# Optimization experiments

Hardware: AMD Instinct MI355X
Metric: run time of the kernel (lower is better)

Reference implementation:

```python
import jax, jax.numpy as jnp
import numpy as np

THRESH = 0.5
DECAY = 0.2
N_NODES = 39
T = 2000
K_HOPS = 3


def setup_inputs() -> dict:
    key = jax.random.key(0)
    ks = jax.random.split(key, 10)
    x = jax.random.normal(ks[0], (N_NODES, 2, T), dtype=jnp.float32)
    edge_index = jax.random.randint(ks[1], (2, 156), 0, N_NODES)
    # TAGConv(2, 64, K=3): (K+1) bias-free hop weights + single bias
    W_conv = jax.random.normal(ks[2], (K_HOPS + 1, 2, 64), dtype=jnp.float32) * 0.3
    b_conv = jax.random.normal(ks[3], (64,), dtype=jnp.float32) * 0.05
    W1 = jax.random.normal(ks[4], (N_NODES * 64, 128), dtype=jnp.float32) * 0.02
    b1 = jax.random.normal(ks[5], (128,), dtype=jnp.float32) * 0.02
    W2 = jax.random.normal(ks[6], (128, 256), dtype=jnp.float32) * 0.08
    b2 = jax.random.normal(ks[7], (256,), dtype=jnp.float32) * 0.02
    W3 = jax.random.normal(ks[8], (256, 36), dtype=jnp.float32) * 0.06
    b3 = jax.random.normal(ks[9], (36,), dtype=jnp.float32) * 0.02
    return {"x": x, "edge_index": edge_index, "W_conv": W_conv, "b_conv": b_conv,
            "W1": W1, "b1": b1, "W2": W2, "b2": b2, "W3": W3, "b3": b3}


def _norm_adj(edge_index, dtype):
    # PyG gcn_norm without self loops: A_hat = D^-1/2 A D^-1/2, message flows row->col
    row, col = edge_index[0], edge_index[1]
    A = jnp.zeros((N_NODES, N_NODES), dtype).at[col, row].add(1.0)
    deg = A.sum(axis=1)
    dinv = jnp.where(deg > 0, deg ** -0.5, 0.0).astype(dtype)
    return dinv[:, None] * A * dinv[None, :]


def reference(x, edge_index, W_conv, b_conv, W1, b1, W2, b2, W3, b3):
    A_hat = _norm_adj(edge_index, x.dtype)

    def spike(m):
        return (m > THRESH).astype(m.dtype)

    def step(carry, xt):
        c1m, c1s, h1m, h1s, h2m, h2s, h3m, h3s, acc = carry
        # TAGConv: sum_k (A_hat^k xt) @ W_k + bias   [39,64]
        h = xt
        conv = h @ W_conv[0]
        for k in range(1, K_HOPS + 1):
            h = A_hat @ h
            conv = conv + h @ W_conv[k]
        conv = conv + b_conv
        c1m = c1m * DECAY * (1.0 - c1s) + conv
        c1s = spike(c1m)
        f = c1s.reshape(-1)  # [2496]
        h1m = h1m * DECAY * (1.0 - h1s) + f @ W1 + b1
        h1s = spike(h1m)
        h2m = h2m * DECAY * (1.0 - h2s) + h1s @ W2 + b2
        h2s = spike(h2m)
        h3m = h3m * DECAY * (1.0 - h3s) + h2s @ W3 + b3
        h3s = spike(h3m)
        return (c1m, c1s, h1m, h1s, h2m, h2s, h3m, h3s, acc + h3s), None

    z = lambda s: jnp.zeros(s, x.dtype)
    init = (z((N_NODES, 64)), z((N_NODES, 64)), z((128,)), z((128,)),
            z((256,)), z((256,)), z((36,)), z((36,)), z((36,)))
    xs = jnp.moveaxis(x, -1, 0)  # [T, 39, 2]
    carry, _ = jax.lax.scan(step, init, xs)
    return carry[-1] / x.shape[-1]
```

## Files before the change

kernel.cpp:

```cpp
#include <hip/hip_runtime.h>

#define T 2000
#define K1N 2496
#define K2 4992
#define TL 48
#define WL 16
#define NCHB 42
#define MAXNZ 24

using short8 = __attribute__((ext_vector_type(8))) short;
using floatx4 = __attribute__((ext_vector_type(4))) float;

__device__ __forceinline__ unsigned bf16_rne(float v) {
    unsigned u = __float_as_uint(v);
    return (u + 0x7FFFu + ((u >> 16) & 1u)) >> 16;
}
__device__ __forceinline__ unsigned packhl(float w) {
    unsigned hi = bf16_rne(w);
    float r = w - __uint_as_float(hi << 16);
    unsigned lo = bf16_rne(r);
    return (hi & 0xFFFFu) | (lo << 16);
}

template<int LEN, bool WRITE>
__device__ __forceinline__ void subtile(
        const float* __restrict__ x, unsigned char* __restrict__ FS,
        float* bufA, float* bufB, float* feat,
        const float2* alist, const int* nnzr,
        int tid, int i0, int iloc, int n, bool vn,
        int ts, const float* wv, float bias, float& m, float& s) {
    constexpr int GC = LEN / 8;
    for (int e = tid; e < 78 * LEN; e += 256) {
        int r = e / LEN, tt = e - r * LEN;
        int t = ts + tt;
        bufA[r * TL + tt] = (t < T) ? x[r * T + t] : 0.f;
    }
    __syncthreads();
    for (int e = tid; e < 8 * LEN; e += 256) {
        int lr = e / LEN, tt = e - lr * LEN;
        int gr = i0 * 2 + lr;
        float v = (gr < 78) ? bufA[gr * TL + tt] : 0.f;
        feat[(((lr >> 1) * TL) + tt) * 8 + (lr & 1)] = v;
    }
    for (int e = tid; e < 78 * GC; e += 256) {
        int r = e / GC, g = e - r * GC;
        int ii = r >> 1, c = r & 1;
        float acc[8];
        #pragma unroll
        for (int u = 0; u < 8; ++u) acc[u] = 0.f;
        int nz = nnzr[ii];
        const float2* lp = &alist[ii * MAXNZ];
        int cg = c * (TL * 4) + g * 32;
        for (int q = 0; q < nz; ++q) {
            float2 av = lp[q];
            const float* xp = (const float*)((const char*)bufA + (__float_as_int(av.y) + cg));
            float a = av.x;
            float4 x0 = *(const float4*)xp;
            float4 x1 = *(const float4*)(xp + 4);
            acc[0] += a * x0.x; acc[1] += a * x0.y; acc[2] += a * x0.z; acc[3] += a * x0.w;
            acc[4] += a * x1.x; acc[5] += a * x1.y; acc[6] += a * x1.z; acc[7] += a * x1.w;
        }
        float* dp = &bufB[r * TL + g * 8];
        *(float4*)dp = *(float4*)&acc[0];
        *(float4*)(dp + 4) = *(float4*)&acc[4];
    }
    __syncthreads();
    for (int e = tid; e < 8 * LEN; e += 256) {
        int lr = e / LEN, tt = e - lr * LEN;
        int gr = i0 * 2 + lr;
        float v = (gr < 78) ? bufB[gr * TL + tt] : 0.f;
        feat[(((lr >> 1) * TL) + tt) * 8 + 2 + (lr & 1)] = v;
    }
    for (int e = tid; e < 78 * GC; e += 256) {
        int r = e / GC, g = e - r * GC;
        int ii = r >> 1, c = r & 1;
        float acc[8];
        #pragma unroll
        for (int u = 0; u < 8; ++u) acc[u] = 0.f;
        int nz = nnzr[ii];
        const float2* lp = &alist[ii * MAXNZ];
        int cg = c * (TL * 4) + g * 32;
        for (int q = 0; q < nz; ++q) {
            float2 av = lp[q];
            const float* xp = (const float*)((const char*)bufB + (__float_as_int(av.y) + cg));
            float a = av.x;
            float4 x0 = *(const float4*)xp;
            float4 x1 = *(const float4*)(xp + 4);
            acc[0] += a * x0.x; acc[1] += a * x0.y; acc[2] += a * x0.z; acc[3] += a * x0.w;
            acc[4] += a * x1.x; acc[5] += a * x1.y; acc[6] += a * x1.z; acc[7] += a * x1.w;
        }
        float* dp = &bufA[r * TL + g * 8];
        *(float4*)dp = *(float4*)&acc[0];
        *(float4*)(dp + 4) = *(float4*)&acc[4];
    }
    __syncthreads();
    for (int e = tid; e < 8 * LEN; e += 256) {
        int lr = e / LEN, tt = e - lr * LEN;
        int gr = i0 * 2 + lr;
        float v = (gr < 78) ? bufA[gr * TL + tt] : 0.f;
        feat[(((lr >> 1) * TL) + tt) * 8 + 4 + (lr & 1)] = v;
    }
    for (int e = tid; e < 8 * GC; e += 256) {
        int lr = e / GC, g = e - lr * GC;
        int gi = i0 + (lr >> 1), c = lr & 1, il = lr >> 1;
        float acc[8];
        #pragma unroll
        for (int u = 0; u < 8; ++u) acc[u] = 0.f;
        if (gi < 39) {
            int nz = nnzr[gi];
            const float2* lp = &alist[gi * MAXNZ];
            int cg = c * (TL * 4) + g * 32;
            for (int q = 0; q < nz; ++q) {
                float2 av = lp[q];
                const float* xp = (const float*)((const char*)bufA + (__float_as_int(av.y) + cg));
                float a = av.x;
                float4 x0 = *(const float4*)xp;
                float4 x1 = *(const float4*)(xp + 4);
                acc[0] += a * x0.x; acc[1] += a * x0.y; acc[2] += a * x0.z; acc[3] += a * x0.w;
                acc[4] += a * x1.x; acc[5] += a * x1.y; acc[6] += a * x1.z; acc[7] += a * x1.w;
            }
        }
        #pragma unroll
        for (int u = 0; u < 8; ++u)
            feat[((il * TL) + g * 8 + u) * 8 + 6 + c] = acc[u];
    }
    __syncthreads();
    for (int tg = 0; tg < LEN; tg += 8) {
        float4 f0a[8], f1a[8];
        #pragma unroll
        for (int u = 0; u < 8; ++u) {
            const float4* fp = (const float4*)&feat[((iloc * TL) + tg + u) * 8];
            f0a[u] = fp[0];
            f1a[u] = fp[1];
        }
        #pragma unroll
        for (int u = 0; u < 8; ++u) {
            float acc = 0.f;
            acc += wv[0] * f0a[u].x; acc += wv[1] * f0a[u].y;
            acc += wv[2] * f0a[u].z; acc += wv[3] * f0a[u].w;
            acc += wv[4] * f1a[u].x; acc += wv[5] * f1a[u].y;
            acc += wv[6] * f1a[u].z; acc += wv[7] * f1a[u].w;
            float v = acc + bias;
            m = m * 0.2f * (1.f - s) + v;
            s = (m > 0.5f) ? 1.f : 0.f;
            if (WRITE && vn) {
                int t = ts + tg + u;
                if (t < T) FS[t * K1N + n] = (unsigned char)(s != 0.f);
            }
        }
    }
    __syncthreads();
}

__global__ __launch_bounds__(256) void conv_scan(const float* __restrict__ x,
        const int* __restrict__ ei, const float* __restrict__ Wc,
        const float* __restrict__ bc, unsigned char* __restrict__ FS,
        const float* __restrict__ W1, unsigned* __restrict__ W1t,
        float* __restrict__ out) {
    __shared__ float ah[1560];
    __shared__ float2 alist[39 * MAXNZ];
    __shared__ int nnzr[40];
    __shared__ float bufA[78 * TL];
    __shared__ float bufB[78 * TL];
    __shared__ float feat[4 * TL * 8];
    int tid = threadIdx.x;
    int nb = blockIdx.x, ch = blockIdx.y;
    int bl = ch * 10 + nb;

    if (bl == 0 && tid < 36) out[tid] = 0.f;

    for (int u = tid; u < 1521; u += 256) ah[u] = 0.f;
    __syncthreads();
    if (tid < 156) atomicAdd(&ah[ei[156 + tid] * 39 + ei[tid]], 1.f);
    __syncthreads();
    if (tid < 39) {
        float d = 0.f;
        for (int u = 0; u < 39; ++u) d += ah[tid * 39 + u];
        ah[1521 + tid] = (d > 0.f) ? (1.f / sqrtf(d)) : 0.f;
    }
    __syncthreads();
    for (int u = tid; u < 1521; u += 256) {
        int i = u / 39, j = u - i * 39;
        ah[u] = (ah[1521 + i] * ah[u]) * ah[1521 + j];
    }
    __syncthreads();
    if (tid < 39) {
        int cnt = 0;
        for (int m = 0; m < 39; ++m) {
            float v = ah[tid * 39 + m];
            if (v != 0.f && cnt < MAXNZ) {
                alist[tid * MAXNZ + cnt] = make_float2(v, __int_as_float((2 * m) * TL * 4));
                ++cnt;
            }
        }
        nnzr[tid] = cnt;
    }
    __syncthreads();

    int t0 = ch * TL;
    int i0 = nb * 4;
    int iloc = tid >> 6, j = tid & 63;
    int n = nb * 256 + tid;
    bool vn = (i0 + iloc) < 39;
    float wv[8], bias;
    #pragma unroll
    for (int q = 0; q < 8; ++q) wv[q] = Wc[q * 64 + j];
    bias = bc[j];
    float m = 0.f, s = 0.f;

    if (t0 >= WL)
        subtile<WL, false>(x, FS, bufA, bufB, feat, alist, nnzr,
                           tid, i0, iloc, n, vn, t0 - WL, wv, bias, m, s);
    subtile<TL, true>(x, FS, bufA, bufB, feat, alist, nnzr,
                      tid, i0, iloc, n, vn, t0, wv, bias, m, s);

    const int total = 128 * K1N;
    for (int f = bl * 256 + tid; f < total; f += 420 * 256) {
        int k = f >> 7, jj = f & 127;
        W1t[jj * K1N + k] = packhl(W1[f]);
    }
}

__global__ __launch_bounds__(256) void gemm1(const unsigned char* __restrict__ FS,
        const short* __restrict__ W1t, float* __restrict__ F1p) {
    __shared__ short As[32 * 72];
    __shared__ short Ws[128 * 72];
    int tid = threadIdx.x;
    int t0 = blockIdx.x * 32;
    int ks = blockIdx.y;
    int lane = tid & 63, wvi = tid >> 6;
    int j0 = wvi * 32;
    int row = lane & 15, quad = lane >> 4;
    floatx4 a00 = {0.f, 0.f, 0.f, 0.f};
    floatx4 a01 = a00, a10 = a00, a11 = a00;
    int kb = ks * 416, kb2 = ks * 832;
    int sm = tid >> 3, sb4 = (tid & 7) * 4;
    int gt = t0 + sm;
    int jjv[4], kov[4];
    #pragma unroll
    for (int u = 0; u < 4; ++u) {
        int aid = u * 256 + tid;
        jjv[u] = aid >> 3;
        kov[u] = (aid & 7) * 8;
    }
    unsigned u4 = 0;
    short8 wr0, wr1, wr2, wr3;
    if (gt < T) u4 = *(const unsigned*)&FS[gt * K1N + kb + sb4];
    wr0 = *(const short8*)&W1t[jjv[0] * K2 + kb2 + kov[0]];
    wr1 = *(const short8*)&W1t[jjv[1] * K2 + kb2 + kov[1]];
    wr2 = *(const short8*)&W1t[jjv[2] * K2 + kb2 + kov[2]];
    wr3 = *(const short8*)&W1t[jjv[3] * K2 + kb2 + kov[3]];
    for (int c = 0; c < 13; ++c) {
        uint4 dd;
        dd.x = (u4 & 0x000000FFu) ? 0x3F803F80u : 0u;
        dd.y = (u4 & 0x0000FF00u) ? 0x3F803F80u : 0u;
        dd.z = (u4 & 0x00FF0000u) ? 0x3F803F80u : 0u;
        dd.w = (u4 & 0xFF000000u) ? 0x3F803F80u : 0u;
        *(uint4*)&As[sm * 72 + sb4 * 2] = dd;
        *(short8*)&Ws[jjv[0] * 72 + kov[0]] = wr0;
        *(short8*)&Ws[jjv[1] * 72 + kov[1]] = wr1;
        *(short8*)&Ws[jjv[2] * 72 + kov[2]] = wr2;
        *(short8*)&Ws[jjv[3] * 72 + kov[3]] = wr3;
        __syncthreads();
        unsigned u4n = 0;
        short8 wn0, wn1, wn2, wn3;
        if (c < 12) {
            if (gt < T) u4n = *(const unsigned*)&FS[gt * K1N + kb + (c + 1) * 32 + sb4];
            wn0 = *(const short8*)&W1t[jjv[0] * K2 + kb2 + (c + 1) * 64 + kov[0]];
            wn1 = *(const short8*)&W1t[jjv[1] * K2 + kb2 + (c + 1) * 64 + kov[1]];
            wn2 = *(const short8*)&W1t[jjv[2] * K2 + kb2 + (c + 1) * 64 + kov[2]];
            wn3 = *(const short8*)&W1t[jjv[3] * K2 + kb2 + (c + 1) * 64 + kov[3]];
        }
        #pragma unroll
        for (int sh = 0; sh < 2; ++sh) {
            int k0 = sh * 32 + quad * 8;
            short8 fa0 = *(const short8*)&As[row * 72 + k0];
            short8 fa1 = *(const short8*)&As[(row + 16) * 72 + k0];
            short8 fb0 = *(const short8*)&Ws[(j0 + row) * 72 + k0];
            short8 fb1 = *(const short8*)&Ws[(j0 + 16 + row) * 72 + k0];
            a00 = __builtin_amdgcn_mfma_f32_16x16x32_bf16(fa0, fb0, a00, 0, 0, 0);
            a01 = __builtin_amdgcn_mfma_f32_16x16x32_bf16(fa0, fb1, a01, 0, 0, 0);
            a10 = __builtin_amdgcn_mfma_f32_16x16x32_bf16(fa1, fb0, a10, 0, 0, 0);
            a11 = __builtin_amdgcn_mfma_f32_16x16x32_bf16(fa1, fb1, a11, 0, 0, 0);
        }
        __syncthreads();
        if (c < 12) { u4 = u4n; wr0 = wn0; wr1 = wn1; wr2 = wn2; wr3 = wn3; }
    }
    #pragma unroll
    for (int r = 0; r < 4; ++r) {
        int m0 = quad * 4 + r;
        int t = t0 + m0;
        if (t < T) {
            F1p[t * 768 + ks * 128 + j0 + row] = a00[r];
            F1p[t * 768 + ks * 128 + j0 + 16 + row] = a01[r];
        }
        int t2 = t0 + 16 + m0;
        if (t2 < T) {
            F1p[t2 * 768 + ks * 128 + j0 + row] = a10[r];
            F1p[t2 * 768 + ks * 128 + j0 + 16 + row] = a11[r];
        }
    }
}

__global__ __launch_bounds__(256) void h1_gemm2(const float* __restrict__ F1p,
        const float* __restrict__ b1, const float* __restrict__ W2,
        float* __restrict__ G2) {
    __shared__ float AT[128 * 8];
    int tid = threadIdx.x;
    int t0 = blockIdx.x * 8;
    if (tid < 128) {
        int n = tid;
        int hs = t0 - 16; if (hs < 0) hs = 0;
        float b = b1[n];
        float m = 0.f, s = 0.f;
        for (int tg = hs; tg < t0 + 8; tg += 4) {
            float vb[4][6];
            #pragma unroll
            for (int u = 0; u < 4; ++u)
                #pragma unroll
                for (int q = 0; q < 6; ++q)
                    vb[u][q] = F1p[(tg + u) * 768 + q * 128 + n];
            #pragma unroll
            for (int u = 0; u < 4; ++u) {
                float v = 0.f;
                #pragma unroll
                for (int q = 0; q < 6; ++q) v += vb[u][q];
                v += b;
                m = m * 0.2f * (1.f - s) + v;
                s = (m > 0.5f) ? 1.f : 0.f;
                int t = tg + u;
                if (t >= t0) AT[n * 8 + (t - t0)] = s;
            }
        }
    }
    __syncthreads();
    int j = tid;
    float acc[8] = {0.f};
    #pragma unroll 4
    for (int k = 0; k < 128; ++k) {
        float w = W2[k * 256 + j];
        float4 q0 = *(const float4*)&AT[k * 8 + 0];
        float4 q1 = *(const float4*)&AT[k * 8 + 4];
        acc[0] += q0.x * w; acc[1] += q0.y * w; acc[2] += q0.z * w; acc[3] += q0.w * w;
        acc[4] += q1.x * w; acc[5] += q1.y * w; acc[6] += q1.z * w; acc[7] += q1.w * w;
    }
    #pragma unroll
    for (int tt = 0; tt < 8; ++tt) G2[(t0 + tt) * 256 + j] = acc[tt];
}

__global__ __launch_bounds__(256) void tail(const float* __restrict__ G2,
        const float* __restrict__ b2, const float* __restrict__ W3,
        const float* __restrict__ b3, float* __restrict__ out) {
    __shared__ float w3t[36 * 260];
    __shared__ unsigned char S2[52 * 260];
    __shared__ float G3[52 * 36];
    int tid = threadIdx.x;
    int t0 = blockIdx.x * 25;
    int gs = t0 - 25; if (gs < 0) gs = 0;
    int hs = gs - 25; if (hs < 0) hs = 0;
    int L3 = t0 + 25 - gs;
    #pragma unroll
    for (int u = 0; u < 9; ++u) {
        int f = u * 1024 + tid * 4;
        float4 wq = *(const float4*)&W3[f];
        int k0 = f / 36, j0 = f - k0 * 36;
        float wv[4] = {wq.x, wq.y, wq.z, wq.w};
        #pragma unroll
        for (int q = 0; q < 4; ++q) {
            int k = (j0 + q >= 36) ? k0 + 1 : k0;
            int jj = (j0 + q >= 36) ? (j0 + q - 36) : (j0 + q);
            w3t[jj * 260 + k] = wv[q];
        }
    }
    {
        int n = tid;
        float b = b2[n];
        float m = 0.f, s = 0.f;
        for (int base = hs; base < t0 + 25; base += 25) {
            float vb[25];
            #pragma unroll
            for (int u = 0; u < 25; ++u) vb[u] = G2[(base + u) * 256 + n];
            #pragma unroll
            for (int u = 0; u < 25; ++u) {
                float v = vb[u] + b;
                m = m * 0.2f * (1.f - s) + v;
                s = (m > 0.5f) ? 1.f : 0.f;
                int t = base + u;
                if (t >= gs) S2[(t - gs) * 260 + n] = (unsigned char)(s != 0.f);
            }
        }
    }
    __syncthreads();
    for (int e = tid; e < 36 * 13; e += 256) {
        int jj = e / 13, g = e - (e / 13) * 13;
        int tb = g * 4;
        if (tb >= L3) continue;
        float ac0 = 0.f, ac1 = 0.f, ac2 = 0.f, ac3 = 0.f;
        const unsigned char* r0 = &S2[tb * 260];
        for (int k = 0; k < 256; k += 4) {
            float4 w = *(const float4*)&w3t[jj * 260 + k];
            uchar4 q0 = *(const uchar4*)&r0[k];
            uchar4 q1 = *(const uchar4*)&r0[260 + k];
            uchar4 q2 = *(const uchar4*)&r0[520 + k];
            uchar4 q3 = *(const uchar4*)&r0[780 + k];
            ac0 += (float)q0.x * w.x + (float)q0.y * w.y + (float)q0.z * w.z + (float)q0.w * w.w;
            ac1 += (float)q1.x * w.x + (float)q1.y * w.y + (float)q1.z * w.z + (float)q1.w * w.w;
            ac2 += (float)q2.x * w.x + (float)q2.y * w.y + (float)q2.z * w.z + (float)q2.w * w.w;
            ac3 += (float)q3.x * w.x + (float)q3.y * w.y + (float)q3.z * w.z + (float)q3.w * w.w;
        }
        G3[tb * 36 + jj] = ac0;
        if (tb + 1 < L3) G3[(tb + 1) * 36 + jj] = ac1;
        if (tb + 2 < L3) G3[(tb + 2) * 36 + jj] = ac2;
        if (tb + 3 < L3) G3[(tb + 3) * 36 + jj] = ac3;
    }
    __syncthreads();
    if (tid < 36) {
        int n = tid;
        float b = b3[n];
        float m = 0.f, s = 0.f;
        int cnt = 0;
        for (int t = gs; t < t0 + 25; ++t) {
            float v = G3[(t - gs) * 36 + n] + b;
            m = m * 0.2f * (1.f - s) + v;
            s = (m > 0.5f) ? 1.f : 0.f;
            if (t >= t0) cnt += (s != 0.f) ? 1 : 0;
        }
        atomicAdd(&out[n], (float)cnt * 0.0005f);
    }
}

extern "C" void kernel_launch(void* const* d_in, const int* in_sizes, int n_in,
                              void* d_out, int out_size, void* d_ws, size_t ws_size,
                              hipStream_t stream) {
    const float* x  = (const float*)d_in[0];
    const int*   ei = (const int*)d_in[1];
    const float* Wc = (const float*)d_in[2];
    const float* bc = (const float*)d_in[3];
    const float* W1 = (const float*)d_in[4];
    const float* b1 = (const float*)d_in[5];
    const float* W2 = (const float*)d_in[6];
    const float* b2 = (const float*)d_in[7];
    const float* W3 = (const float*)d_in[8];
    const float* b3 = (const float*)d_in[9];
    float* out = (float*)d_out;

    float* w = (float*)d_ws;
    float* F1p = w;                       w += (size_t)T * 768;
    float* G2  = w;                       w += (size_t)T * 256;
    unsigned* W1t = (unsigned*)w;         w += 128 * K1N;
    unsigned char* FS = (unsigned char*)w;

    conv_scan<<<dim3(10, NCHB), 256, 0, stream>>>(x, ei, Wc, bc, FS, W1, W1t, out);
    gemm1<<<dim3(63, 6), 256, 0, stream>>>(FS, (const short*)W1t, F1p);
    h1_gemm2<<<250, 256, 0, stream>>>(F1p, b1, W2, G2);
    tail<<<80, 256, 0, stream>>>(G2, b2, W3, b3, out);
}
```

Before: 145.6 us.

## Split graph-hop computation into separate kernel, removing redundant per-block hop recomputation

```diff
diff --git a/kernel.cpp b/kernel.cpp
--- a/kernel.cpp
+++ b/kernel.cpp
@@ -6,6 +6,7 @@
 #define TL 48
 #define WL 16
 #define NCHB 42
+#define TLA 8
 #define MAXNZ 24
 
 using short8 = __attribute__((ext_vector_type(8))) short;
@@ -22,35 +23,69 @@
     return (hi & 0xFFFFu) | (lo << 16);
 }
 
-template<int LEN, bool WRITE>
-__device__ __forceinline__ void subtile(
-        const float* __restrict__ x, unsigned char* __restrict__ FS,
-        float* bufA, float* bufB, float* feat,
-        const float2* alist, const int* nnzr,
-        int tid, int i0, int iloc, int n, bool vn,
-        int ts, const float* wv, float bias, float& m, float& s) {
-    constexpr int GC = LEN / 8;
-    for (int e = tid; e < 78 * LEN; e += 256) {
-        int r = e / LEN, tt = e - r * LEN;
-        int t = ts + tt;
-        bufA[r * TL + tt] = (t < T) ? x[r * T + t] : 0.f;
-    }
-    __syncthreads();
-    for (int e = tid; e < 8 * LEN; e += 256) {
-        int lr = e / LEN, tt = e - lr * LEN;
-        int gr = i0 * 2 + lr;
-        float v = (gr < 78) ? bufA[gr * TL + tt] : 0.f;
-        feat[(((lr >> 1) * TL) + tt) * 8 + (lr & 1)] = v;
-    }
-    for (int e = tid; e < 78 * GC; e += 256) {
-        int r = e / GC, g = e - r * GC;
+__global__ __launch_bounds__(256) void hops(const float* __restrict__ x,
+        const int* __restrict__ ei, float* __restrict__ Fg,
+        const float* __restrict__ W1, unsigned* __restrict__ W1t,
+        float* __restrict__ out) {
+    __shared__ float ah[1560];
+    __shared__ float2 alist[39 * MAXNZ];
+    __shared__ int nnzr[40];
+    __shared__ float bufA[78 * TLA];
+    __shared__ float bufB[78 * TLA];
+    __shared__ float feat[39 * TLA * 8];
+    int tid = threadIdx.x;
+    int bl = blockIdx.x;
+    int ts = bl * TLA;
+
+    if (bl == 0 && tid < 36) out[tid] = 0.f;
+
+    for (int u = tid; u < 1521; u += 256) ah[u] = 0.f;
+    __syncthreads();
+    if (tid < 156) atomicAdd(&ah[ei[156 + tid] * 39 + ei[tid]], 1.f);
+    __syncthreads();
+    if (tid < 39) {
+        float d = 0.f;
+        for (int u = 0; u < 39; ++u) d += ah[tid * 39 + u];
+        ah[1521 + tid] = (d > 0.f) ? (1.f / sqrtf(d)) : 0.f;
+    }
+    __syncthreads();
+    for (int u = tid; u < 1521; u += 256) {
+        int i = u / 39, j = u - i * 39;
+        ah[u] = (ah[1521 + i] * ah[u]) * ah[1521 + j];
+    }
+    __syncthreads();
+    if (tid < 39) {
+        int cnt = 0;
+        for (int m = 0; m < 39; ++m) {
+            float v = ah[tid * 39 + m];
+            if (v != 0.f && cnt < MAXNZ) {
+                alist[tid * MAXNZ + cnt] = make_float2(v, __int_as_float((2 * m) * TLA * 4));
+                ++cnt;
+            }
+        }
+        nnzr[tid] = cnt;
+    }
+    __syncthreads();
+
+    for (int e = tid; e < 78 * TLA; e += 256) {
+        int r = e / TLA, tt = e - r * TLA;
+        bufA[r * TLA + tt] = x[r * T + ts + tt];
+    }
+    __syncthreads();
+
+    for (int e = tid; e < 78 * TLA; e += 256) {
+        int r = e / TLA, tt = e - r * TLA;
+        feat[((r >> 1) * TLA + tt) * 8 + (r & 1)] = bufA[r * TLA + tt];
+    }
+    for (int e = tid; e < 78; e += 256) {
+        int r = e;
         int ii = r >> 1, c = r & 1;
         float acc[8];
         #pragma unroll
         for (int u = 0; u < 8; ++u) acc[u] = 0.f;
         int nz = nnzr[ii];
         const float2* lp = &alist[ii * MAXNZ];
-        int cg = c * (TL * 4) + g * 32;
+        int cg = c * (TLA * 4);
         for (int q = 0; q < nz; ++q) {
             float2 av = lp[q];
             const float* xp = (const float*)((const char*)bufA + (__float_as_int(av.y) + cg));
@@ -60,26 +95,25 @@
             acc[0] += a * x0.x; acc[1] += a * x0.y; acc[2] += a * x0.z; acc[3] += a * x0.w;
             acc[4] += a * x1.x; acc[5] += a * x1.y; acc[6] += a * x1.z; acc[7] += a * x1.w;
         }
-        float* dp = &bufB[r * TL + g * 8];
+        float* dp = &bufB[r * TLA];
         *(float4*)dp = *(float4*)&acc[0];
         *(float4*)(dp + 4) = *(float4*)&acc[4];
     }
     __syncthreads();
-    for (int e = tid; e < 8 * LEN; e += 256) {
-        int lr = e / LEN, tt = e - lr * LEN;
-        int gr = i0 * 2 + lr;
-        float v = (gr < 78) ? bufB[gr * TL + tt] : 0.f;
-        feat[(((lr >> 1) * TL) + tt) * 8 + 2 + (lr & 1)] = v;
-    }
-    for (int e = tid; e < 78 * GC; e += 256) {
-        int r = e / GC, g = e - r * GC;
+
+    for (int e = tid; e < 78 * TLA; e += 256) {
+        int r = e / TLA, tt = e - r * TLA;
+        feat[((r >> 1) * TLA + tt) * 8 + 2 + (r & 1)] = bufB[r * TLA + tt];
+    }
+    for (int e = tid; e < 78; e += 256) {
+        int r = e;
         int ii = r >> 1, c = r & 1;
         float acc[8];
         #pragma unroll
         for (int u = 0; u < 8; ++u) acc[u] = 0.f;
         int nz = nnzr[ii];
         const float2* lp = &alist[ii * MAXNZ];
-        int cg = c * (TL * 4) + g * 32;
+        int cg = c * (TLA * 4);
         for (int q = 0; q < nz; ++q) {
             float2 av = lp[q];
             const float* xp = (const float*)((const char*)bufB + (__float_as_int(av.y) + cg));
@@ -89,47 +123,90 @@
             acc[0] += a * x0.x; acc[1] += a * x0.y; acc[2] += a * x0.z; acc[3] += a * x0.w;
             acc[4] += a * x1.x; acc[5] += a * x1.y; acc[6] += a * x1.z; acc[7] += a * x1.w;
         }
-        float* dp = &bufA[r * TL + g * 8];
+        float* dp = &bufA[r * TLA];
         *(float4*)dp = *(float4*)&acc[0];
         *(float4*)(dp + 4) = *(float4*)&acc[4];
     }
     __syncthreads();
-    for (int e = tid; e < 8 * LEN; e += 256) {
-        int lr = e / LEN, tt = e - lr * LEN;
-        int gr = i0 * 2 + lr;
-        float v = (gr < 78) ? bufA[gr * TL + tt] : 0.f;
-        feat[(((lr >> 1) * TL) + tt) * 8 + 4 + (lr & 1)] = v;
-    }
-    for (int e = tid; e < 8 * GC; e += 256) {
-        int lr = e / GC, g = e - lr * GC;
-        int gi = i0 + (lr >> 1), c = lr & 1, il = lr >> 1;
+
+    for (int e = tid; e < 78 * TLA; e += 256) {
+        int r = e / TLA, tt = e - r * TLA;
+        feat[((r >> 1) * TLA + tt) * 8 + 4 + (r & 1)] = bufA[r * TLA + tt];
+    }
+    for (int e = tid; e < 78; e += 256) {
+        int r = e;
+        int ii = r >> 1, c = r & 1;
         float acc[8];
         #pragma unroll
         for (int u = 0; u < 8; ++u) acc[u] = 0.f;
-        if (gi < 39) {
-            int nz = nnzr[gi];
-            const float2* lp = &alist[gi * MAXNZ];
-            int cg = c * (TL * 4) + g * 32;
-            for (int q = 0; q < nz; ++q) {
-                float2 av = lp[q];
-                const float* xp = (const float*)((const char*)bufA + (__float_as_int(av.y) + cg));
-                float a = av.x;
-                float4 x0 = *(const float4*)xp;
-                float4 x1 = *(const float4*)(xp + 4);
-                acc[0] += a * x0.x; acc[1] += a * x0.y; acc[2] += a * x0.z; acc[3] += a * x0.w;
-                acc[4] += a * x1.x; acc[5] += a * x1.y; acc[6] += a * x1.z; acc[7] += a * x1.w;
-            }
+        int nz = nnzr[ii];
+        const float2* lp = &alist[ii * MAXNZ];
+        int cg = c * (TLA * 4);
+        for (int q = 0; q < nz; ++q) {
+            float2 av = lp[q];
+            const float* xp = (const float*)((const char*)bufA + (__float_as_int(av.y) + cg));
+            float a = av.x;
+            float4 x0 = *(const float4*)xp;
+            float4 x1 = *(const float4*)(xp + 4);
+            acc[0] += a * x0.x; acc[1] += a * x0.y; acc[2] += a * x0.z; acc[3] += a * x0.w;
+            acc[4] += a * x1.x; acc[5] += a * x1.y; acc[6] += a * x1.z; acc[7] += a * x1.w;
         }
         #pragma unroll
         for (int u = 0; u < 8; ++u)
-            feat[((il * TL) + g * 8 + u) * 8 + 6 + c] = acc[u];
-    }
-    __syncthreads();
-    for (int tg = 0; tg < LEN; tg += 8) {
+            feat[(ii * TLA + u) * 8 + 6 + c] = acc[u];
+    }
+    __syncthreads();
+
+    for (int e = tid; e < 39 * TLA * 2; e += 256) {
+        int idx = e >> 1, half = e & 1;
+        int n = idx / TLA, tt = idx - n * TLA;
+        *(float4*)&Fg[((size_t)n * T + ts + tt) * 8 + half * 4] =
+            *(const float4*)&feat[idx * 8 + half * 4];
+    }
+
+    const int total = 128 * K1N;
+    for (int f = bl * 256 + tid; f < total; f += 250 * 256) {
+        int k = f >> 7, jj = f & 127;
+        W1t[jj * K1N + k] = packhl(W1[f]);
+    }
+}
+
+__global__ __launch_bounds__(256) void scan_c1(const float* __restrict__ Fg,
+        const float* __restrict__ Wc, const float* __restrict__ bc,
+        unsigned char* __restrict__ FS) {
+    __shared__ float featL[4 * 64 * 8];
+    int tid = threadIdx.x;
+    int nb = blockIdx.x, ch = blockIdx.y;
+    int t0 = ch * TL;
+    int hs = t0 - WL; if (hs < 0) hs = 0;
+    int ncol = (t0 + TL) - hs;
+    int i0 = nb * 4;
+
+    for (int e = tid; e < 4 * ncol * 2; e += 256) {
+        int idx = e >> 1, half = e & 1;
+        int il = idx / ncol, cc = idx - il * ncol;
+        int gn = i0 + il, t = hs + cc;
+        float4 v = make_float4(0.f, 0.f, 0.f, 0.f);
+        if (gn < 39 && t < T)
+            v = *(const float4*)&Fg[((size_t)gn * T + t) * 8 + half * 4];
+        *(float4*)&featL[(il * 64 + cc) * 8 + half * 4] = v;
+    }
+    __syncthreads();
+
+    int iloc = tid >> 6, j = tid & 63;
+    int n = nb * 256 + tid;
+    bool vn = (i0 + iloc) < 39;
+    float wv[8], bias;
+    #pragma unroll
+    for (int q = 0; q < 8; ++q) wv[q] = Wc[q * 64 + j];
+    bias = bc[j];
+    float m = 0.f, s = 0.f;
+
+    for (int tg = 0; tg < ncol; tg += 8) {
         float4 f0a[8], f1a[8];
         #pragma unroll
         for (int u = 0; u < 8; ++u) {
-            const float4* fp = (const float4*)&feat[((iloc * TL) + tg + u) * 8];
+            const float4* fp = (const float4*)&featL[((iloc * 64) + tg + u) * 8];
             f0a[u] = fp[0];
             f1a[u] = fp[1];
         }
@@ -143,81 +220,9 @@
             float v = acc + bias;
             m = m * 0.2f * (1.f - s) + v;
             s = (m > 0.5f) ? 1.f : 0.f;
-            if (WRITE && vn) {
-                int t = ts + tg + u;
-                if (t < T) FS[t * K1N + n] = (unsigned char)(s != 0.f);
-            }
-        }
-    }
-    __syncthreads();
-}
-
-__global__ __launch_bounds__(256) void conv_scan(const float* __restrict__ x,
-        const int* __restrict__ ei, const float* __restrict__ Wc,
-        const float* __restrict__ bc, unsigned char* __restrict__ FS,
-        const float* __restrict__ W1, unsigned* __restrict__ W1t,
-        float* __restrict__ out) {
-    __shared__ float ah[1560];
-    __shared__ float2 alist[39 * MAXNZ];
-    __shared__ int nnzr[40];
-    __shared__ float bufA[78 * TL];
-    __shared__ float bufB[78 * TL];
-    __shared__ float feat[4 * TL * 8];
-    int tid = threadIdx.x;
-    int nb = blockIdx.x, ch = blockIdx.y;
-    int bl = ch * 10 + nb;
-
-    if (bl == 0 && tid < 36) out[tid] = 0.f;
-
-    for (int u = tid; u < 1521; u += 256) ah[u] = 0.f;
-    __syncthreads();
-    if (tid < 156) atomicAdd(&ah[ei[156 + tid] * 39 + ei[tid]], 1.f);
-    __syncthreads();
-    if (tid < 39) {
-        float d = 0.f;
-        for (int u = 0; u < 39; ++u) d += ah[tid * 39 + u];
-        ah[1521 + tid] = (d > 0.f) ? (1.f / sqrtf(d)) : 0.f;
-    }
-    __syncthreads();
-    for (int u = tid; u < 1521; u += 256) {
-        int i = u / 39, j = u - i * 39;
-        ah[u] = (ah[1521 + i] * ah[u]) * ah[1521 + j];
-    }
-    __syncthreads();
-    if (tid < 39) {
-        int cnt = 0;
-        for (int m = 0; m < 39; ++m) {
-            float v = ah[tid * 39 + m];
-            if (v != 0.f && cnt < MAXNZ) {
-                alist[tid * MAXNZ + cnt] = make_float2(v, __int_as_float((2 * m) * TL * 4));
-                ++cnt;
-            }
-        }
-        nnzr[tid] = cnt;
-    }
-    __syncthreads();
-
-    int t0 = ch * TL;
-    int i0 = nb * 4;
-    int iloc = tid >> 6, j = tid & 63;
-    int n = nb * 256 + tid;
-    bool vn = (i0 + iloc) < 39;
-    float wv[8], bias;
-    #pragma unroll
-    for (int q = 0; q < 8; ++q) wv[q] = Wc[q * 64 + j];
-    bias = bc[j];
-    float m = 0.f, s = 0.f;
-
-    if (t0 >= WL)
-        subtile<WL, false>(x, FS, bufA, bufB, feat, alist, nnzr,
-                           tid, i0, iloc, n, vn, t0 - WL, wv, bias, m, s);
-    subtile<TL, true>(x, FS, bufA, bufB, feat, alist, nnzr,
-                      tid, i0, iloc, n, vn, t0, wv, bias, m, s);
-
-    const int total = 128 * K1N;
-    for (int f = bl * 256 + tid; f < total; f += 420 * 256) {
-        int k = f >> 7, jj = f & 127;
-        W1t[jj * K1N + k] = packhl(W1[f]);
+            int t = hs + tg + u;
+            if (vn && t >= t0 && t < T) FS[t * K1N + n] = (unsigned char)(s != 0.f);
+        }
     }
 }
 
@@ -447,10 +452,12 @@
     float* w = (float*)d_ws;
     float* F1p = w;                       w += (size_t)T * 768;
     float* G2  = w;                       w += (size_t)T * 256;
+    float* Fg  = w;                       w += (size_t)39 * T * 8;
     unsigned* W1t = (unsigned*)w;         w += 128 * K1N;
     unsigned char* FS = (unsigned char*)w;
 
-    conv_scan<<<dim3(10, NCHB), 256, 0, stream>>>(x, ei, Wc, bc, FS, W1, W1t, out);
+    hops<<<250, 256, 0, stream>>>(x, ei, Fg, W1, W1t, out);
+    scan_c1<<<dim3(10, NCHB), 256, 0, stream>>>(Fg, Wc, bc, FS);
     gemm1<<<dim3(63, 6), 256, 0, stream>>>(FS, (const short*)W1t, F1p);
     h1_gemm2<<<250, 256, 0, stream>>>(F1p, b1, W2, G2);
     tail<<<80, 256, 0, stream>>>(G2, b2, W3, b3, out);
```

After: 138.3 us. -5.0%, faster.
